# Optimization experiments

Hardware: AMD Instinct MI355X
Metric: run time of the kernel (lower is better)

The kernel has to match this reference:

```python
import jax, jax.numpy as jnp
import numpy as np

B, SA, SB, H, D = 1, 2048, 512, 24, 128
DIM = H * D
EPS = 1e-6


def rms_norm(x, w):
    # fp32 variance as in the torch module (inputs already fp32 here)
    var = jnp.mean(jnp.square(x.astype(jnp.float32)), axis=-1, keepdims=True)
    y = (x * jax.lax.rsqrt(var + EPS)).astype(x.dtype)
    return y * w


def apply_rope(x, freqs):
    # x: [B,H,S,D]; freqs: [1,1,S,D/2,2,2]
    x_ = x.astype(jnp.float32).reshape(*x.shape[:-1], -1, 1, 2)  # [B,H,S,D/2,1,2]
    out = freqs[..., 0] * x_[..., 0] + freqs[..., 1] * x_[..., 1]  # [B,H,S,D/2,2]
    return out.reshape(x.shape).astype(x.dtype)


def qkv_split(x, W, b):
    # x: [B,S,DIM] -> q,k,v each [B,H,S,D]; chunk(3,dim=1) on 3H axis == major-3 split
    qkv = (x @ W + b).reshape(x.shape[0], x.shape[1], 3, H, D)
    qkv = jnp.transpose(qkv, (2, 0, 3, 1, 4))  # [3,B,H,S,D]
    return qkv[0], qkv[1], qkv[2]


def setup_inputs():
    key = jax.random.key(0)
    ks = jax.random.split(key, 8)
    s = 0.02
    return {
        "hidden_states_a": jax.random.normal(ks[0], (B, SA, DIM), jnp.float32),
        "hidden_states_b": jax.random.normal(ks[1], (B, SB, DIM), jnp.float32),
        "image_rotary_emb": jax.random.normal(ks[2], (1, 1, SA + SB, D // 2, 2, 2), jnp.float32),
        "Wqkv_a": jax.random.normal(ks[3], (DIM, 3 * DIM), jnp.float32) * s,
        "bqkv_a": jnp.zeros((3 * DIM,), jnp.float32),
        "Wqkv_b": jax.random.normal(ks[4], (DIM, 3 * DIM), jnp.float32) * s,
        "bqkv_b": jnp.zeros((3 * DIM,), jnp.float32),
        "wq_a": jnp.ones((D,), jnp.float32),
        "wk_a": jnp.ones((D,), jnp.float32),
        "wq_b": jnp.ones((D,), jnp.float32),
        "wk_b": jnp.ones((D,), jnp.float32),
        "Wout_a": jax.random.normal(ks[5], (DIM, DIM), jnp.float32) * s,
        "bout_a": jnp.zeros((DIM,), jnp.float32),
        "Wout_b": jax.random.normal(ks[6], (DIM, DIM), jnp.float32) * s,
        "bout_b": jnp.zeros((DIM,), jnp.float32),
    }


def reference(hidden_states_a, hidden_states_b, image_rotary_emb,
              Wqkv_a, bqkv_a, Wqkv_b, bqkv_b,
              wq_a, wk_a, wq_b, wk_b,
              Wout_a, bout_a, Wout_b, bout_b):
    q_a, k_a, v_a = qkv_split(hidden_states_a, Wqkv_a, bqkv_a)
    q_a, k_a = rms_norm(q_a, wq_a), rms_norm(k_a, wk_a)
    q_b, k_b, v_b = qkv_split(hidden_states_b, Wqkv_b, bqkv_b)
    q_b, k_b = rms_norm(q_b, wq_b), rms_norm(k_b, wk_b)

    q = jnp.concatenate([q_b, q_a], axis=2)
    k = jnp.concatenate([k_b, k_a], axis=2)
    v = jnp.concatenate([v_b, v_a], axis=2)
    q, k = apply_rope(q, image_rotary_emb), apply_rope(k, image_rotary_emb)

    scale = 1.0 / jnp.sqrt(jnp.asarray(D, q.dtype))
    scores = jnp.einsum("bhqd,bhkd->bhqk", q, k) * scale
    attn = jax.nn.softmax(scores, axis=-1)
    out = jnp.einsum("bhqk,bhkd->bhqd", attn, v)
    out = jnp.transpose(out, (0, 2, 1, 3)).reshape(B, SA + SB, DIM)

    out_b, out_a = out[:, :SB], out[:, SB:]
    hidden_states_a = out_a @ Wout_a + bout_a
    hidden_states_b = out_b @ Wout_b + bout_b
    return hidden_states_a, hidden_states_b
```

## Files before the change

kernel.cpp:

```cpp
#include <hip/hip_runtime.h>
#include <hip/hip_bf16.h>


typedef __attribute__((ext_vector_type(8))) short s16x8;
typedef __attribute__((ext_vector_type(8))) unsigned short u16x8;
typedef __attribute__((ext_vector_type(4))) float f32x4;
typedef __attribute__((ext_vector_type(16))) float f32x16;

#define DEV static __device__ __forceinline__

#define S_TOT 2560
#define DIMC 3072
#define NQKV 9216

DEV unsigned short f2bf(float f) {
  union { float f; unsigned u; } v; v.f = f;
  return (unsigned short)((v.u + 0x7fffu + ((v.u >> 16) & 1u)) >> 16);
}
DEV float bf2f(unsigned short h) {
  union { unsigned u; float f; } v; v.u = ((unsigned)h) << 16;
  return v.f;
}
DEV void gload16(const void* g, void* l) {
  __builtin_amdgcn_global_load_lds((__attribute__((address_space(1))) void*)g,
                                   (__attribute__((address_space(3))) void*)l,
                                   16, 0, 0);
}
template <int N>
DEV void wait_vm() { asm volatile("s_waitcnt vmcnt(%0)" :: "n"(N) : "memory"); }
DEV float exp2_fast(float x) {
#if __has_builtin(__builtin_amdgcn_exp2f)
  return __builtin_amdgcn_exp2f(x);
#else
  return __expf(x * 0.69314718056f);
#endif
}
template <int CTRL>
DEV float dppf(float x) {
  return __int_as_float(__builtin_amdgcn_update_dpp(0, __float_as_int(x), CTRL, 0xf, 0xf, true));
}
DEV float rowmax16(float x) {
  x = fmaxf(x, dppf<0xB1>(x));
  x = fmaxf(x, dppf<0x4E>(x));
  x = fmaxf(x, dppf<0x141>(x));
  x = fmaxf(x, dppf<0x140>(x));
  return x;
}
DEV float rowsum16(float x) {
  x += dppf<0xB1>(x);
  x += dppf<0x4E>(x);
  x += dppf<0x141>(x);
  x += dppf<0x140>(x);
  return x;
}

DEV void tile_map(int t, int mgrid, int* m, int* n) {
  int sg = t >> 4, loc = t & 15;
  int mgs = mgrid >> 2;
  int mg = sg % mgs, ng = sg / mgs;
  *m = mg * 4 + (loc & 3);
  *n = ng * 4 + (loc >> 2);
}


__global__ __launch_bounds__(256) void cvt_both(const float* __restrict__ Xa,
                                                const float* __restrict__ Xb,
                                                unsigned short* __restrict__ Oa,
                                                unsigned short* __restrict__ Ob,
                                                int n8a, int n8b) {
  int i = blockIdx.x * 256 + threadIdx.x;
  const float* in; unsigned short* out;
  if (i < n8a) { in = Xa; out = Oa; }
  else { i -= n8a; if (i >= n8b) return; in = Xb; out = Ob; }
  const float4* p = (const float4*)(in + (size_t)i * 8);
  float4 a = p[0], b = p[1];
  u16x8 u;
  u[0] = f2bf(a.x); u[1] = f2bf(a.y); u[2] = f2bf(a.z); u[3] = f2bf(a.w);
  u[4] = f2bf(b.x); u[5] = f2bf(b.y); u[6] = f2bf(b.z); u[7] = f2bf(b.w);
  *(u16x8*)(out + (size_t)i * 8) = u;
}

__global__ __launch_bounds__(256) void transpose_all(
    const float* __restrict__ Wqa, const float* __restrict__ Wqb,
    const float* __restrict__ Woa, const float* __restrict__ Wob,
    unsigned short* __restrict__ Tqa, unsigned short* __restrict__ Tqb,
    unsigned short* __restrict__ Toa, unsigned short* __restrict__ Tob) {
  __shared__ float tile[64][65];
  int id = blockIdx.x;
  const float* W; unsigned short* WT; int N, ncols;
  if (id < 6912)        { W = Wqa; WT = Tqa; N = NQKV; ncols = 144; }
  else if (id < 13824)  { W = Wqb; WT = Tqb; N = NQKV; ncols = 144; id -= 6912; }
  else if (id < 16128)  { W = Woa; WT = Toa; N = DIMC; ncols = 48;  id -= 13824; }
  else                  { W = Wob; WT = Tob; N = DIMC; ncols = 48;  id -= 16128; }
  const int t = threadIdx.x;
  const int n0 = (id % ncols) * 64, k0 = (id / ncols) * 64;
#pragma unroll
  for (int rep = 0; rep < 4; ++rep) {
    int idx = rep * 256 + t;
    int r = idx >> 4, c4 = (idx & 15) * 4;
    float4 v = *(const float4*)&W[(size_t)(k0 + r) * N + n0 + c4];
    tile[r][c4] = v.x; tile[r][c4 + 1] = v.y; tile[r][c4 + 2] = v.z; tile[r][c4 + 3] = v.w;
  }
  __syncthreads();
#pragma unroll
  for (int rep = 0; rep < 2; ++rep) {
    int idx = rep * 256 + t;
    int j = idx >> 3, i0 = (idx & 7) * 8;
    u16x8 u;
#pragma unroll
    for (int i = 0; i < 8; i++) u[i] = f2bf(tile[i0 + i][j]);
    *(u16x8*)&WT[(size_t)(n0 + j) * DIMC + k0 + i0] = u;
  }
}


struct StageSmem {
  unsigned short A[128 * 64];
  unsigned short B[128 * 64];
};

DEV void stage_tile(const char* A, const char* B, StageSmem* s, int kt, int tid) {
  const int row_s = tid >> 3;
  const int kbp = (tid & 7) * 16;
#pragma unroll
  for (int st = 0; st < 4; ++st) {
    int row = st * 32 + row_s;
    int kb = kbp ^ ((row & 7) << 4);
    gload16(A + (size_t)row * (DIMC * 2) + kt * 128 + kb, (char*)s->A + st * 4096 + tid * 16);
    gload16(B + (size_t)row * (DIMC * 2) + kt * 128 + kb, (char*)s->B + st * 4096 + tid * 16);
  }
}

DEV void compute_tile(const StageSmem* s, int wr, int wc, int lh, int ll,
                      f32x4 (&acc)[4][4]) {
#pragma unroll
  for (int ks = 0; ks < 2; ++ks) {
    s16x8 a[4], b[4];
#pragma unroll
    for (int f = 0; f < 4; ++f) {
      int ar = wr * 64 + f * 16 + ll;
      a[f] = *(const s16x8*)((const char*)s->A + ar * 128 +
                             ((ks * 64 + lh * 16) ^ ((ar & 7) << 4)));
      int br = wc * 64 + f * 16 + ll;
      b[f] = *(const s16x8*)((const char*)s->B + br * 128 +
                             ((ks * 64 + lh * 16) ^ ((br & 7) << 4)));
    }
#pragma unroll
    for (int i = 0; i < 4; i++)
#pragma unroll
      for (int j = 0; j < 4; j++)
        acc[i][j] = __builtin_amdgcn_mfma_f32_16x16x32_bf16(a[i], b[j], acc[i][j], 0, 0, 0);
  }
}

DEV void gemm_core_sb(const unsigned short* __restrict__ Ap,
                      const unsigned short* __restrict__ Bp,
                      StageSmem* s, int tid, f32x4 (&acc)[4][4]) {
  const int wave = tid >> 6, lane = tid & 63;
  const int wr = wave >> 1, wc = wave & 1;
  const int lh = lane >> 4, ll = lane & 15;
  for (int kt = 0; kt < 48; ++kt) {
    stage_tile((const char*)Ap, (const char*)Bp, s, kt, tid);
    __syncthreads();
    compute_tile(s, wr, wc, lh, ll, acc);
    __syncthreads();
  }
}

DEV void gemm_core_db(const unsigned short* __restrict__ Ap,
                      const unsigned short* __restrict__ Bp,
                      StageSmem (&sm)[2], int tid, f32x4 (&acc)[4][4]) {
  const int wave = tid >> 6, lane = tid & 63;
  const int wr = wave >> 1, wc = wave & 1;
  const int lh = lane >> 4, ll = lane & 15;

  stage_tile((const char*)Ap, (const char*)Bp, &sm[0], 0, tid);
  __syncthreads();
  for (int kt = 0; kt < 48; ++kt) {
    if (kt + 1 < 48)
      stage_tile((const char*)Ap, (const char*)Bp, &sm[(kt + 1) & 1], kt + 1, tid);
    compute_tile(&sm[kt & 1], wr, wc, lh, ll, acc);
    __syncthreads();
  }
}


union QkvSmem {
  StageSmem st;
  unsigned short ctile[128 * 136];
  char pad[49152];
};

__global__ __launch_bounds__(256, 2) void qkv_gemm(
    const unsigned short* __restrict__ X0, const unsigned short* __restrict__ X1,
    const unsigned short* __restrict__ W0, const unsigned short* __restrict__ W1,
    const float* __restrict__ b0, const float* __restrict__ b1,
    const float* __restrict__ wqa, const float* __restrict__ wka,
    const float* __restrict__ wqb, const float* __restrict__ wkb,
    const float* __restrict__ freqs,
    unsigned short* __restrict__ Qb, unsigned short* __restrict__ Kb,
    unsigned short* __restrict__ Vt, int nt0) {
  __shared__ QkvSmem sm;
  const int tid = threadIdx.x;

  const int chunk = gridDim.x >> 3;
  const int nid = ((int)blockIdx.x & 7) * chunk + ((int)blockIdx.x >> 3);
  const int strm = (nid >= nt0) ? 1 : 0;
  const int t = strm ? nid - nt0 : nid;
  int mt, nt;
  tile_map(t, strm ? 4 : 16, &mt, &nt);
  const int m0 = mt * 128, n0 = nt * 128;
  const unsigned short* Xp = (strm ? X1 : X0) + (size_t)m0 * DIMC;
  const unsigned short* Wp = (strm ? W1 : W0) + (size_t)n0 * DIMC;
  const float* biasp = (strm ? b1 : b0);
  const int s_off = strm ? 0 : 512;

  f32x4 acc[4][4] = {};
  gemm_core_sb(Xp, Wp, &sm.st, tid, acc);

  {
    const int wave = tid >> 6, lane = tid & 63;
    const int wr = wave >> 1, wc = wave & 1, lh = lane >> 4, ll = lane & 15;
#pragma unroll
    for (int fn = 0; fn < 4; ++fn) {
      int c = wc * 64 + fn * 16 + ll;
      float bv = biasp[n0 + c];
#pragma unroll
      for (int fm = 0; fm < 4; ++fm)
#pragma unroll
        for (int j = 0; j < 4; j++) {
          int r = wr * 64 + fm * 16 + lh * 4 + j;
          sm.ctile[r * 136 + c] = f2bf(acc[fm][fn][j] + bv);
        }
    }
  }
  __syncthreads();

  const int qkv_idx = nt / 24;
  const int head = nt % 24;

  if (qkv_idx == 2) {
    const int sg0 = s_off + m0;
#pragma unroll
    for (int half = 0; half < 2; ++half) {
      int d = half * 64 + (tid >> 2);
      int t0 = (tid & 3) * 32;
      size_t obase = (size_t)(head * 128 + d) * S_TOT + sg0 + t0;
#pragma unroll
      for (int v = 0; v < 4; ++v) {
        u16x8 u;
#pragma unroll
        for (int i = 0; i < 8; i++) u[i] = sm.ctile[(t0 + v * 8 + i) * 136 + d];
        *(u16x8*)&Vt[obase + v * 8] = u;
      }
    }
  } else {
    const float* wn = (qkv_idx == 0) ? (strm ? wqb : wqa) : (strm ? wkb : wka);
    unsigned short* Ob = (qkv_idx == 0) ? Qb : Kb;
    const int row = tid >> 1, half = tid & 1;
    const int sg = s_off + m0 + row;
    float x[64];
    float ss = 0.f;
#pragma unroll
    for (int i = 0; i < 64; i++) {
      float v = bf2f(sm.ctile[row * 136 + half * 64 + i]);
      x[i] = v; ss += v * v;
    }
    ss += __shfl_xor(ss, 1);
    const float rn = rsqrtf(ss * (1.f / 128.f) + 1e-6f);
    const float* fr = freqs + (size_t)sg * 256 + half * 128;
    unsigned short o[64];
#pragma unroll
    for (int p = 0; p < 32; ++p) {
      float w0 = wn[half * 64 + 2 * p], w1 = wn[half * 64 + 2 * p + 1];
      float y0 = x[2 * p] * rn * w0, y1 = x[2 * p + 1] * rn * w1;
      float f00 = fr[p * 4], f01 = fr[p * 4 + 1], f10 = fr[p * 4 + 2], f11 = fr[p * 4 + 3];
      o[2 * p] = f2bf(f00 * y0 + f01 * y1);
      o[2 * p + 1] = f2bf(f10 * y0 + f11 * y1);
    }
    size_t ob = ((size_t)head * S_TOT + sg) * 128 + half * 64;
#pragma unroll
    for (int v = 0; v < 8; ++v) {
      u16x8 u;
#pragma unroll
      for (int i = 0; i < 8; i++) u[i] = o[v * 8 + i];
      *(u16x8*)&Ob[ob + v * 8] = u;
    }
  }
}


__global__ __launch_bounds__(256, 2) void out_gemm(
    const unsigned short* __restrict__ A0, const unsigned short* __restrict__ A1,
    const unsigned short* __restrict__ W0, const unsigned short* __restrict__ W1,
    const float* __restrict__ b0, const float* __restrict__ b1,
    float* __restrict__ C0, float* __restrict__ C1, int nt0) {
  __shared__ StageSmem sm[2];
  const int tid = threadIdx.x;
  const int chunk = gridDim.x >> 3;
  const int nid = ((int)blockIdx.x & 7) * chunk + ((int)blockIdx.x >> 3);
  const int strm = (nid >= nt0) ? 1 : 0;
  const int t = strm ? nid - nt0 : nid;
  int mt, nt;
  tile_map(t, strm ? 4 : 16, &mt, &nt);
  const int m0 = mt * 128, n0 = nt * 128;
  const unsigned short* Ap = (strm ? A1 : A0) + (size_t)m0 * DIMC;
  const unsigned short* Wp = (strm ? W1 : W0) + (size_t)n0 * DIMC;
  const float* bias = strm ? b1 : b0;
  float* C = strm ? C1 : C0;

  f32x4 acc[4][4] = {};
  gemm_core_db(Ap, Wp, sm, tid, acc);
  const int wave = tid >> 6, lane = tid & 63;
  const int wr = wave >> 1, wc = wave & 1, lh = lane >> 4, ll = lane & 15;
#pragma unroll
  for (int fn = 0; fn < 4; ++fn) {
    int c = n0 + wc * 64 + fn * 16 + ll;
    float bv = bias[c];
#pragma unroll
    for (int fm = 0; fm < 4; ++fm)
#pragma unroll
      for (int j = 0; j < 4; j++) {
        int r = m0 + wr * 64 + fm * 16 + lh * 4 + j;
        C[(size_t)r * DIMC + c] = acc[fm][fn][j] + bv;
      }
  }
}


__global__ __launch_bounds__(256, 2) void attn_k(
    const unsigned short* __restrict__ Qb, const unsigned short* __restrict__ Kb,
    const unsigned short* __restrict__ Vt, unsigned short* __restrict__ AO) {
  __shared__ alignas(128) unsigned short Ks[2][64 * 128];
  __shared__ alignas(128) unsigned short Vs[128 * 64];
  __shared__ alignas(128) unsigned short Ps[4][32 * 72];
  __shared__ float tabA[4][32];
  __shared__ float tabL[4][32];

  const int tid = threadIdx.x, w = tid >> 6, lane = tid & 63;
  const int lh = lane >> 4, ll16 = lane & 15;
  const int ll31 = lane & 31, hi = lane >> 5;
  const int wgid = blockIdx.x;
  const int nid = (wgid & 7) * 60 + (wgid >> 3);
  const int h = nid / 20, qt = nid % 20;
  const float C = 0.12751744f;

  s16x8 qf[2][4];
#pragma unroll
  for (int rb = 0; rb < 2; rb++) {
    size_t qbase = ((size_t)h * S_TOT + qt * 128 + w * 32 + rb * 16 + ll16) * 128;
#pragma unroll
    for (int ks = 0; ks < 4; ks++) qf[rb][ks] = *(const s16x8*)&Qb[qbase + ks * 32 + lh * 8];
  }

  float m2[2][4], l_r[2][4];
  f32x16 o[4] = {};
#pragma unroll
  for (int rb = 0; rb < 2; rb++)
#pragma unroll
    for (int j = 0; j < 4; j++) { m2[rb][j] = -1e30f; l_r[rb][j] = 0.f; }

  const unsigned short* Kh = Kb + (size_t)h * S_TOT * 128;
  const unsigned short* Vh = Vt + (size_t)h * 128 * S_TOT;
  unsigned short* Pw = &Ps[w][0];

  {
#pragma unroll
    for (int st = 0; st < 4; ++st) {
      int row = st * 16 + (tid >> 4);
      int col = ((tid & 15) * 16) ^ ((row & 7) << 4);
      gload16((const char*)(Kh + (size_t)row * 128) + col,
              (char*)&Ks[0][0] + st * 4096 + tid * 16);
    }
  }

  int cur = 0;
  for (int kt = 0; kt < 40; ++kt) {
    wait_vm<0>();
    __builtin_amdgcn_s_barrier();
    {
      const int k0 = kt * 64;
#pragma unroll
      for (int st = 0; st < 4; ++st) {
        int row = st * 32 + (tid >> 3);
        int col = ((tid & 7) * 16) ^ ((row & 7) << 4);
        gload16((const char*)(Vh + (size_t)row * S_TOT + k0) + col,
                (char*)Vs + st * 4096 + tid * 16);
      }
    }
    if (kt + 1 < 40) {
      const unsigned short* Kn = Kh + (size_t)(kt + 1) * 64 * 128;
#pragma unroll
      for (int st = 0; st < 4; ++st) {
        int row = st * 16 + (tid >> 4);
        int col = ((tid & 15) * 16) ^ ((row & 7) << 4);
        gload16((const char*)(Kn + (size_t)row * 128) + col,
                (char*)&Ks[cur ^ 1][0] + st * 4096 + tid * 16);
      }
    }

    const char* Kc = (const char*)&Ks[cur][0];
    f32x4 sc[2][4] = {};
#pragma unroll
    for (int kb = 0; kb < 4; kb++) {
      int krow = kb * 16 + ll16;
      const char* kr = Kc + krow * 256;
      int swz = (krow & 7) << 4;
#pragma unroll
      for (int ks = 0; ks < 4; ks++) {
        s16x8 bf = *(const s16x8*)(kr + ((ks * 64 + lh * 16) ^ swz));
        sc[0][kb] = __builtin_amdgcn_mfma_f32_16x16x32_bf16(qf[0][ks], bf, sc[0][kb], 0, 0, 0);
        sc[1][kb] = __builtin_amdgcn_mfma_f32_16x16x32_bf16(qf[1][ks], bf, sc[1][kb], 0, 0, 0);
      }
    }

    float pmax[2][4];
#pragma unroll
    for (int rb = 0; rb < 2; rb++)
#pragma unroll
      for (int j = 0; j < 4; j++) {
        float v = fmaxf(fmaxf(sc[rb][0][j], sc[rb][1][j]), fmaxf(sc[rb][2][j], sc[rb][3][j]));
        pmax[rb][j] = rowmax16(v) * C;
      }
    bool need = false;
#pragma unroll
    for (int rb = 0; rb < 2; rb++)
#pragma unroll
      for (int j = 0; j < 4; j++) need |= (pmax[rb][j] > m2[rb][j] + 8.0f);
    if (__any(need)) {
#pragma unroll
      for (int rb = 0; rb < 2; rb++)
#pragma unroll
        for (int j = 0; j < 4; j++) {
          float mn = fmaxf(m2[rb][j], pmax[rb][j]);
          float al = exp2_fast(m2[rb][j] - mn);
          m2[rb][j] = mn;
          l_r[rb][j] *= al;
          if (ll16 == 0) tabA[w][rb * 16 + lh * 4 + j] = al;
        }
#pragma unroll
      for (int reg = 0; reg < 16; reg++) {
        int cr = (reg & 3) + 8 * (reg >> 2) + 4 * hi;
        float alv = tabA[w][cr];
        o[0][reg] *= alv; o[1][reg] *= alv; o[2][reg] *= alv; o[3][reg] *= alv;
      }
    }
#pragma unroll
    for (int rb = 0; rb < 2; rb++) {
      float ps0 = 0.f, ps1 = 0.f, ps2 = 0.f, ps3 = 0.f;
#pragma unroll
      for (int kb = 0; kb < 4; kb++) {
        float p0 = exp2_fast(sc[rb][kb][0] * C - m2[rb][0]);
        float p1 = exp2_fast(sc[rb][kb][1] * C - m2[rb][1]);
        float p2 = exp2_fast(sc[rb][kb][2] * C - m2[rb][2]);
        float p3 = exp2_fast(sc[rb][kb][3] * C - m2[rb][3]);
        ps0 += p0; ps1 += p1; ps2 += p2; ps3 += p3;
        int rbase = (rb * 16 + lh * 4);
        Pw[(rbase + 0) * 72 + kb * 16 + ll16] = f2bf(p0);
        Pw[(rbase + 1) * 72 + kb * 16 + ll16] = f2bf(p1);
        Pw[(rbase + 2) * 72 + kb * 16 + ll16] = f2bf(p2);
        Pw[(rbase + 3) * 72 + kb * 16 + ll16] = f2bf(p3);
      }
      l_r[rb][0] += rowsum16(ps0);
      l_r[rb][1] += rowsum16(ps1);
      l_r[rb][2] += rowsum16(ps2);
      l_r[rb][3] += rowsum16(ps3);
    }

    if (kt + 1 < 40) wait_vm<16>(); else wait_vm<0>();
    __builtin_amdgcn_s_barrier();

#pragma unroll
    for (int kstep = 0; kstep < 4; kstep++) {
      s16x8 pa = *(const s16x8*)((const char*)Pw + ll31 * 144 + kstep * 32 + hi * 16);
#pragma unroll
      for (int dblk = 0; dblk < 4; dblk++) {
        int vrow = dblk * 32 + ll31;
        s16x8 vb = *(const s16x8*)((const char*)Vs + vrow * 128 +
                                   ((kstep * 32 + hi * 16) ^ ((vrow & 7) << 4)));
        o[dblk] = __builtin_amdgcn_mfma_f32_32x32x16_bf16(pa, vb, o[dblk], 0, 0, 0);
      }
    }
    cur ^= 1;
  }

  if (ll16 == 0) {
#pragma unroll
    for (int rb = 0; rb < 2; rb++)
#pragma unroll
      for (int j = 0; j < 4; j++) tabL[w][rb * 16 + lh * 4 + j] = l_r[rb][j];
  }
#pragma unroll
  for (int reg = 0; reg < 16; reg++) {
    int cr = (reg & 3) + 8 * (reg >> 2) + 4 * hi;
    float inv = 1.0f / tabL[w][cr];
    int srow = qt * 128 + w * 32 + cr;
    size_t base = (size_t)srow * DIMC + h * 128;
#pragma unroll
    for (int dblk = 0; dblk < 4; dblk++)
      AO[base + dblk * 32 + ll31] = f2bf(o[dblk][reg] * inv);
  }
}


extern "C" void kernel_launch(void* const* d_in, const int* in_sizes, int n_in,
                              void* d_out, int out_size, void* d_ws, size_t ws_size,
                              hipStream_t stream) {
  (void)in_sizes; (void)n_in; (void)out_size; (void)ws_size;
  const float* Xa = (const float*)d_in[0];
  const float* Xb = (const float*)d_in[1];
  const float* freqs = (const float*)d_in[2];
  const float* Wqkv_a = (const float*)d_in[3];
  const float* bqkv_a = (const float*)d_in[4];
  const float* Wqkv_b = (const float*)d_in[5];
  const float* bqkv_b = (const float*)d_in[6];
  const float* wq_a = (const float*)d_in[7];
  const float* wk_a = (const float*)d_in[8];
  const float* wq_b = (const float*)d_in[9];
  const float* wk_b = (const float*)d_in[10];
  const float* Wout_a = (const float*)d_in[11];
  const float* bout_a = (const float*)d_in[12];
  const float* Wout_b = (const float*)d_in[13];
  const float* bout_b = (const float*)d_in[14];
  float* out = (float*)d_out;

  char* ws = (char*)d_ws;
  unsigned short* WTa  = (unsigned short*)ws; ws += (size_t)NQKV * DIMC * 2;
  unsigned short* WTb  = (unsigned short*)ws; ws += (size_t)NQKV * DIMC * 2;
  unsigned short* WoTa = (unsigned short*)ws; ws += (size_t)DIMC * DIMC * 2;
  unsigned short* WoTb = (unsigned short*)ws; ws += (size_t)DIMC * DIMC * 2;
  unsigned short* Xa16 = (unsigned short*)ws; ws += (size_t)2048 * DIMC * 2;
  unsigned short* Xb16 = (unsigned short*)ws; ws += (size_t)512 * DIMC * 2;
  unsigned short* Qb   = (unsigned short*)ws; ws += (size_t)24 * S_TOT * 128 * 2;
  unsigned short* Kbf  = (unsigned short*)ws; ws += (size_t)24 * S_TOT * 128 * 2;
  unsigned short* Vt   = (unsigned short*)ws; ws += (size_t)24 * S_TOT * 128 * 2;
  unsigned short* AO   = (unsigned short*)ws; ws += (size_t)S_TOT * DIMC * 2;

  const int n8a = 2048 * DIMC / 8, n8b = 512 * DIMC / 8;
  cvt_both<<<dim3((n8a + n8b) / 256), dim3(256), 0, stream>>>(Xa, Xb, Xa16, Xb16, n8a, n8b);
  transpose_all<<<dim3(18432), dim3(256), 0, stream>>>(Wqkv_a, Wqkv_b, Wout_a, Wout_b,
                                                       WTa, WTb, WoTa, WoTb);

  qkv_gemm<<<dim3(1440), dim3(256), 0, stream>>>(Xa16, Xb16, WTa, WTb, bqkv_a, bqkv_b,
                                                 wq_a, wk_a, wq_b, wk_b, freqs,
                                                 Qb, Kbf, Vt, 1152);

  attn_k<<<dim3(480), dim3(256), 0, stream>>>(Qb, Kbf, Vt, AO);

  out_gemm<<<dim3(480), dim3(256), 0, stream>>>(AO + (size_t)512 * DIMC, AO, WoTa, WoTb,
                                                bout_a, bout_b, out,
                                                out + (size_t)2048 * DIMC, 384);
}
```

Measured before the change: 495.5 us.

## Transpose QK MFMA operands and double-buffer the QKV GEMM stage

The attention kernel swaps the MFMA operand order so each lane owns one query row. Row max and row sum then become in-register reductions plus two cross-lane shuffles instead of four DPP steps per value, and P is written as packed 4-element vectors. The QKV GEMM also moves from the single-buffered core to the existing double-buffered core, overlapping tile staging with compute. The extra LDS for two stage buffers could lower occupancy under the launch bound of two blocks per CU.

```diff
diff --git a/kernel.cpp b/kernel.cpp
--- a/kernel.cpp
+++ b/kernel.cpp
@@ -4,6 +4,7 @@
 
 typedef __attribute__((ext_vector_type(8))) short s16x8;
 typedef __attribute__((ext_vector_type(8))) unsigned short u16x8;
+typedef __attribute__((ext_vector_type(4))) unsigned short u16x4;
 typedef __attribute__((ext_vector_type(4))) float f32x4;
 typedef __attribute__((ext_vector_type(16))) float f32x16;
 
@@ -34,24 +35,6 @@
 #else
   return __expf(x * 0.69314718056f);
 #endif
-}
-template <int CTRL>
-DEV float dppf(float x) {
-  return __int_as_float(__builtin_amdgcn_update_dpp(0, __float_as_int(x), CTRL, 0xf, 0xf, true));
-}
-DEV float rowmax16(float x) {
-  x = fmaxf(x, dppf<0xB1>(x));
-  x = fmaxf(x, dppf<0x4E>(x));
-  x = fmaxf(x, dppf<0x141>(x));
-  x = fmaxf(x, dppf<0x140>(x));
-  return x;
-}
-DEV float rowsum16(float x) {
-  x += dppf<0xB1>(x);
-  x += dppf<0x4E>(x);
-  x += dppf<0x141>(x);
-  x += dppf<0x140>(x);
-  return x;
 }
 
 DEV void tile_map(int t, int mgrid, int* m, int* n) {
@@ -153,20 +136,6 @@
   }
 }
 
-DEV void gemm_core_sb(const unsigned short* __restrict__ Ap,
-                      const unsigned short* __restrict__ Bp,
-                      StageSmem* s, int tid, f32x4 (&acc)[4][4]) {
-  const int wave = tid >> 6, lane = tid & 63;
-  const int wr = wave >> 1, wc = wave & 1;
-  const int lh = lane >> 4, ll = lane & 15;
-  for (int kt = 0; kt < 48; ++kt) {
-    stage_tile((const char*)Ap, (const char*)Bp, s, kt, tid);
-    __syncthreads();
-    compute_tile(s, wr, wc, lh, ll, acc);
-    __syncthreads();
-  }
-}
-
 DEV void gemm_core_db(const unsigned short* __restrict__ Ap,
                       const unsigned short* __restrict__ Bp,
                       StageSmem (&sm)[2], int tid, f32x4 (&acc)[4][4]) {
@@ -186,9 +155,8 @@
 
 
 union QkvSmem {
-  StageSmem st;
+  StageSmem st[2];
   unsigned short ctile[128 * 136];
-  char pad[49152];
 };
 
 __global__ __launch_bounds__(256, 2) void qkv_gemm(
@@ -216,7 +184,7 @@
   const int s_off = strm ? 0 : 512;
 
   f32x4 acc[4][4] = {};
-  gemm_core_sb(Xp, Wp, &sm.st, tid, acc);
+  gemm_core_db(Xp, Wp, sm.st, tid, acc);
 
   {
     const int wave = tid >> 6, lane = tid & 63;
@@ -353,12 +321,10 @@
     for (int ks = 0; ks < 4; ks++) qf[rb][ks] = *(const s16x8*)&Qb[qbase + ks * 32 + lh * 8];
   }
 
-  float m2[2][4], l_r[2][4];
+  float m2[2], l_r[2];
   f32x16 o[4] = {};
-#pragma unroll
-  for (int rb = 0; rb < 2; rb++)
-#pragma unroll
-    for (int j = 0; j < 4; j++) { m2[rb][j] = -1e30f; l_r[rb][j] = 0.f; }
+  m2[0] = m2[1] = -1e30f;
+  l_r[0] = l_r[1] = 0.f;
 
   const unsigned short* Kh = Kb + (size_t)h * S_TOT * 128;
   const unsigned short* Vh = Vt + (size_t)h * 128 * S_TOT;
@@ -409,35 +375,33 @@
 #pragma unroll
       for (int ks = 0; ks < 4; ks++) {
         s16x8 bf = *(const s16x8*)(kr + ((ks * 64 + lh * 16) ^ swz));
-        sc[0][kb] = __builtin_amdgcn_mfma_f32_16x16x32_bf16(qf[0][ks], bf, sc[0][kb], 0, 0, 0);
-        sc[1][kb] = __builtin_amdgcn_mfma_f32_16x16x32_bf16(qf[1][ks], bf, sc[1][kb], 0, 0, 0);
-      }
-    }
-
-    float pmax[2][4];
-#pragma unroll
-    for (int rb = 0; rb < 2; rb++)
-#pragma unroll
-      for (int j = 0; j < 4; j++) {
-        float v = fmaxf(fmaxf(sc[rb][0][j], sc[rb][1][j]), fmaxf(sc[rb][2][j], sc[rb][3][j]));
-        pmax[rb][j] = rowmax16(v) * C;
-      }
-    bool need = false;
-#pragma unroll
-    for (int rb = 0; rb < 2; rb++)
-#pragma unroll
-      for (int j = 0; j < 4; j++) need |= (pmax[rb][j] > m2[rb][j] + 8.0f);
+        sc[0][kb] = __builtin_amdgcn_mfma_f32_16x16x32_bf16(bf, qf[0][ks], sc[0][kb], 0, 0, 0);
+        sc[1][kb] = __builtin_amdgcn_mfma_f32_16x16x32_bf16(bf, qf[1][ks], sc[1][kb], 0, 0, 0);
+      }
+    }
+
+    float pmax[2];
+#pragma unroll
+    for (int rb = 0; rb < 2; rb++) {
+      float v0 = fmaxf(fmaxf(sc[rb][0][0], sc[rb][0][1]), fmaxf(sc[rb][0][2], sc[rb][0][3]));
+      float v1 = fmaxf(fmaxf(sc[rb][1][0], sc[rb][1][1]), fmaxf(sc[rb][1][2], sc[rb][1][3]));
+      float v2 = fmaxf(fmaxf(sc[rb][2][0], sc[rb][2][1]), fmaxf(sc[rb][2][2], sc[rb][2][3]));
+      float v3 = fmaxf(fmaxf(sc[rb][3][0], sc[rb][3][1]), fmaxf(sc[rb][3][2], sc[rb][3][3]));
+      float v = fmaxf(fmaxf(v0, v1), fmaxf(v2, v3));
+      v = fmaxf(v, __shfl_xor(v, 16));
+      v = fmaxf(v, __shfl_xor(v, 32));
+      pmax[rb] = v * C;
+    }
+    bool need = (pmax[0] > m2[0] + 8.0f) | (pmax[1] > m2[1] + 8.0f);
     if (__any(need)) {
 #pragma unroll
-      for (int rb = 0; rb < 2; rb++)
-#pragma unroll
-        for (int j = 0; j < 4; j++) {
-          float mn = fmaxf(m2[rb][j], pmax[rb][j]);
-          float al = exp2_fast(m2[rb][j] - mn);
-          m2[rb][j] = mn;
-          l_r[rb][j] *= al;
-          if (ll16 == 0) tabA[w][rb * 16 + lh * 4 + j] = al;
-        }
+      for (int rb = 0; rb < 2; rb++) {
+        float mn = fmaxf(m2[rb], pmax[rb]);
+        float al = exp2_fast(m2[rb] - mn);
+        m2[rb] = mn;
+        l_r[rb] *= al;
+        if (lane < 16) tabA[w][rb * 16 + lane] = al;
+      }
 #pragma unroll
       for (int reg = 0; reg < 16; reg++) {
         int cr = (reg & 3) + 8 * (reg >> 2) + 4 * hi;
@@ -447,24 +411,21 @@
     }
 #pragma unroll
     for (int rb = 0; rb < 2; rb++) {
-      float ps0 = 0.f, ps1 = 0.f, ps2 = 0.f, ps3 = 0.f;
+      float ps = 0.f;
 #pragma unroll
       for (int kb = 0; kb < 4; kb++) {
-        float p0 = exp2_fast(sc[rb][kb][0] * C - m2[rb][0]);
-        float p1 = exp2_fast(sc[rb][kb][1] * C - m2[rb][1]);
-        float p2 = exp2_fast(sc[rb][kb][2] * C - m2[rb][2]);
-        float p3 = exp2_fast(sc[rb][kb][3] * C - m2[rb][3]);
-        ps0 += p0; ps1 += p1; ps2 += p2; ps3 += p3;
-        int rbase = (rb * 16 + lh * 4);
-        Pw[(rbase + 0) * 72 + kb * 16 + ll16] = f2bf(p0);
-        Pw[(rbase + 1) * 72 + kb * 16 + ll16] = f2bf(p1);
-        Pw[(rbase + 2) * 72 + kb * 16 + ll16] = f2bf(p2);
-        Pw[(rbase + 3) * 72 + kb * 16 + ll16] = f2bf(p3);
-      }
-      l_r[rb][0] += rowsum16(ps0);
-      l_r[rb][1] += rowsum16(ps1);
-      l_r[rb][2] += rowsum16(ps2);
-      l_r[rb][3] += rowsum16(ps3);
+        float p0 = exp2_fast(sc[rb][kb][0] * C - m2[rb]);
+        float p1 = exp2_fast(sc[rb][kb][1] * C - m2[rb]);
+        float p2 = exp2_fast(sc[rb][kb][2] * C - m2[rb]);
+        float p3 = exp2_fast(sc[rb][kb][3] * C - m2[rb]);
+        ps += (p0 + p1) + (p2 + p3);
+        u16x4 pk;
+        pk[0] = f2bf(p0); pk[1] = f2bf(p1); pk[2] = f2bf(p2); pk[3] = f2bf(p3);
+        *(u16x4*)((char*)Pw + (rb * 16 + ll16) * 144 + kb * 32 + lh * 8) = pk;
+      }
+      ps += __shfl_xor(ps, 16);
+      ps += __shfl_xor(ps, 32);
+      l_r[rb] += ps;
     }
 
     if (kt + 1 < 40) wait_vm<16>(); else wait_vm<0>();
@@ -484,11 +445,9 @@
     cur ^= 1;
   }
 
-  if (ll16 == 0) {
-#pragma unroll
-    for (int rb = 0; rb < 2; rb++)
-#pragma unroll
-      for (int j = 0; j < 4; j++) tabL[w][rb * 16 + lh * 4 + j] = l_r[rb][j];
+  if (lane < 16) {
+    tabL[w][lane] = l_r[0];
+    tabL[w][16 + lane] = l_r[1];
   }
 #pragma unroll
   for (int reg = 0; reg < 16; reg++) {
```

New measurement: 448.5 us. -9.5%, faster.
